# Kernel tuning notes

Measured on AMD Instinct MI355X. Metric: run time of the kernel, lower is better.

## Reference

```python
import jax, jax.numpy as jnp
import numpy as np

D_MODEL = 256
N_HEAD = 8
HEAD_DIM = D_MODEL // N_HEAD
N_TOTAL = 24576
B, T = 64, 512


def setup_inputs() -> dict:
    key = jax.random.key(0)
    ks = jax.random.split(key, 12)
    s = 1.0 / np.sqrt(D_MODEL)
    return {
        "x": jax.random.normal(ks[0], (N_TOTAL, D_MODEL), jnp.float32),
        "Wq": jax.random.uniform(ks[1], (D_MODEL, D_MODEL), jnp.float32, -s, s),
        "bq": jax.random.uniform(ks[2], (D_MODEL,), jnp.float32, -s, s),
        "Wk": jax.random.uniform(ks[3], (D_MODEL, D_MODEL), jnp.float32, -s, s),
        "bk": jax.random.uniform(ks[4], (D_MODEL,), jnp.float32, -s, s),
        "Wv": jax.random.uniform(ks[5], (D_MODEL, D_MODEL), jnp.float32, -s, s),
        "bv": jax.random.uniform(ks[6], (D_MODEL,), jnp.float32, -s, s),
        "Wp": jax.random.uniform(ks[7], (D_MODEL, D_MODEL), jnp.float32, -s, s),
        "bp": jax.random.uniform(ks[8], (D_MODEL,), jnp.float32, -s, s),
        "padpack_index": jax.random.randint(ks[9], (B, T), 0, N_TOTAL, jnp.int64 if jax.config.jax_enable_x64 else jnp.int32),
        "padpack_batch": jax.random.randint(ks[10], (B, T), 0, B, jnp.int32),
        "padpack_inverse_index": jax.random.randint(ks[11], (N_TOTAL,), 0, B * T, jnp.int64 if jax.config.jax_enable_x64 else jnp.int32),
    }


def reference(x, Wq, bq, Wk, bk, Wv, bv, Wp, bp, padpack_index, padpack_batch, padpack_inverse_index):
    # gather ragged tokens into packed [B, T, C]
    xp = x[padpack_index]
    # mask: True where packed slots share the same segment id (matches
    # original masked_fill(batch_i == batch_j, -1e9))
    mask = padpack_batch[:, :, None] == padpack_batch[:, None, :]  # [B,T,T]
    # QKV projections (torch Linear: x @ W.T + b), split heads
    def heads(w, b):
        h = xp @ w.T + b
        return h.reshape(B, T, N_HEAD, HEAD_DIM).transpose(0, 2, 1, 3)  # [B,H,T,D]
    q, k, v = heads(Wq, bq), heads(Wk, bk), heads(Wv, bv)
    att = jnp.einsum("bhtd,bhsd->bhts", q, k) * (1.0 / np.sqrt(HEAD_DIM))
    att = jnp.where(mask[:, None], jnp.float32(-1e9), att)
    att = jax.nn.softmax(att, axis=-1)
    y = jnp.einsum("bhts,bhsd->bhtd", att, v)  # [B,H,T,D]
    y = y.transpose(0, 2, 1, 3).reshape(B, T, D_MODEL)
    y = y @ Wp.T + bp
    # scatter back to ragged layout
    return y.reshape(B * T, D_MODEL)[padpack_inverse_index]
```

## Files before the change

### kernel.cpp

```cpp
#include <hip/hip_runtime.h>


typedef __attribute__((ext_vector_type(8))) short short8;
typedef __attribute__((ext_vector_type(4))) short short4_t;
typedef __attribute__((ext_vector_type(4))) float f32x4;

#define N_TOTAL 24576
#define B_ 64
#define T_ 512
#define DM 256
#define NH 8
#define HD 32
#define F3 768

#define QSCALE 0.25503463f
#define VSP 530

__device__ __forceinline__ unsigned short f2bf(float f) {
  unsigned int u = __float_as_uint(f);
  u += 0x7fffu + ((u >> 16) & 1u);
  return (unsigned short)(u >> 16);
}

__device__ __forceinline__ void gl_lds16(const void* g, void* l) {
  __builtin_amdgcn_global_load_lds(
      (const __attribute__((address_space(1))) unsigned int*)g,
      (__attribute__((address_space(3))) unsigned int*)l, 16, 0, 0);
}

__global__ __launch_bounds__(256) void qkv_gemm(
    const float* __restrict__ x, const int* __restrict__ idx,
    const float* __restrict__ Wq, const float* __restrict__ Wk,
    const float* __restrict__ Wv, const float* __restrict__ bq,
    const float* __restrict__ bk, const float* __restrict__ bv,
    unsigned short* __restrict__ QKVp) {
  __shared__ __align__(16) char Asm[8 * 4096];
  __shared__ __align__(16) char Bsm[3 * 8192];
  int tid = threadIdx.x;
  int lane = tid & 63, w = tid >> 6;
  int i = lane & 15, q = lane >> 4;
  int m0 = blockIdx.x * 64;
  int wn = w * 32;
  int csa = q ^ ((i >> 1) & 3);

  int row = tid >> 2, c = tid & 3;
  int cs0 = c ^ ((row >> 1) & 3);
  int brow1 = 64 + row;
  int cs1 = c ^ ((brow1 >> 1) & 3);
  const float* ax = x + (size_t)idx[m0 + row] * DM;

  auto wrow = [&](int f) -> const float* {
    const float* Wb = (f < 256) ? Wq : ((f < 512) ? Wk : Wv);
    return Wb + (size_t)(f & 255) * DM;
  };

  float4 fb[2][2][2];

  auto issueBloads = [&](int g, int par) {
    int p2 = g >> 3, k2 = g & 7;
    const float* s0 = wrow(p2 * 128 + row) + k2 * 32 + cs0 * 8;
    const float* s1 = wrow(p2 * 128 + brow1) + k2 * 32 + cs1 * 8;
    fb[par][0][0] = *(const float4*)(s0);
    fb[par][0][1] = *(const float4*)(s0 + 4);
    fb[par][1][0] = *(const float4*)(s1);
    fb[par][1][1] = *(const float4*)(s1 + 4);
  };
  auto writeB = [&](int g, int par) {
    char* dst = Bsm + (g % 3) * 8192;
    short8 o0, o1;
    float4 l0 = fb[par][0][0], h0 = fb[par][0][1];
    float4 l1 = fb[par][1][0], h1 = fb[par][1][1];
    o0[0] = (short)f2bf(l0.x); o0[1] = (short)f2bf(l0.y);
    o0[2] = (short)f2bf(l0.z); o0[3] = (short)f2bf(l0.w);
    o0[4] = (short)f2bf(h0.x); o0[5] = (short)f2bf(h0.y);
    o0[6] = (short)f2bf(h0.z); o0[7] = (short)f2bf(h0.w);
    o1[0] = (short)f2bf(l1.x); o1[1] = (short)f2bf(l1.y);
    o1[2] = (short)f2bf(l1.z); o1[3] = (short)f2bf(l1.w);
    o1[4] = (short)f2bf(h1.x); o1[5] = (short)f2bf(h1.y);
    o1[6] = (short)f2bf(h1.z); o1[7] = (short)f2bf(h1.w);
    *(short8*)(dst + tid * 16) = o0;
    *(short8*)(dst + (256 + tid) * 16) = o1;
  };

  issueBloads(0, 0);
  issueBloads(1, 1);
#pragma unroll
  for (int k = 0; k < 8; k++) {
    float4 lo = *(const float4*)(ax + k * 32 + cs0 * 8);
    float4 hi = *(const float4*)(ax + k * 32 + cs0 * 8 + 4);
    short8 o;
    o[0] = (short)f2bf(lo.x); o[1] = (short)f2bf(lo.y);
    o[2] = (short)f2bf(lo.z); o[3] = (short)f2bf(lo.w);
    o[4] = (short)f2bf(hi.x); o[5] = (short)f2bf(hi.y);
    o[6] = (short)f2bf(hi.z); o[7] = (short)f2bf(hi.w);
    *(short8*)(Asm + k * 4096 + tid * 16) = o;
  }
  writeB(0, 0);

  f32x4 zf = {0.f, 0.f, 0.f, 0.f};
  f32x4 acc[4][2];
#pragma unroll
  for (int mt = 0; mt < 4; mt++) {
    acc[mt][0] = zf;
    acc[mt][1] = zf;
  }

#pragma unroll 1
  for (int p = 0; p < 6; p++) {
#pragma unroll
    for (int k = 0; k < 8; k++) {
      int g = p * 8 + k;
      asm volatile("s_waitcnt lgkmcnt(0)\ns_barrier" ::: "memory");
      const short* Asb = (const short*)(Asm + k * 4096);
      const short* Bsb = (const short*)(Bsm + (g % 3) * 8192);
      short8 a[4], bfr[2];
#pragma unroll
      for (int mt = 0; mt < 4; mt++)
        a[mt] = *(const short8*)&Asb[(mt * 16 + i) * 32 + csa * 8];
#pragma unroll
      for (int nt = 0; nt < 2; nt++)
        bfr[nt] = *(const short8*)&Bsb[(wn + nt * 16 + i) * 32 + csa * 8];
      if (g + 2 < 48) issueBloads(g + 2, k & 1);
#pragma unroll
      for (int mt = 0; mt < 4; mt++) {
        acc[mt][0] = __builtin_amdgcn_mfma_f32_16x16x32_bf16(a[mt], bfr[0], acc[mt][0], 0, 0, 0);
        acc[mt][1] = __builtin_amdgcn_mfma_f32_16x16x32_bf16(a[mt], bfr[1], acc[mt][1], 0, 0, 0);
      }
      if (g + 1 < 48) writeB(g + 1, (k + 1) & 1);
    }
    float scale = (p < 2) ? QSCALE : 1.0f;
    const float* bb = (p < 2) ? bq : ((p < 4) ? bk : bv);
    int boff = (p < 2) ? 0 : ((p < 4) ? 256 : 512);
#pragma unroll
    for (int nt = 0; nt < 2; nt++) {
      int f = p * 128 + wn + nt * 16 + i;
      float bias = bb[f - boff];
#pragma unroll
      for (int mt = 0; mt < 4; mt++) {
#pragma unroll
        for (int r = 0; r < 4; r++) {
          int token = m0 + mt * 16 + q * 4 + r;
          QKVp[(size_t)token * F3 + f] = f2bf((acc[mt][nt][r] + bias) * scale);
        }
        acc[mt][nt] = zf;
      }
    }
  }
}

__global__ __launch_bounds__(512, 4) void attn_kernel(
    const unsigned short* __restrict__ QKVp, const int* __restrict__ batch,
    const float* __restrict__ Wp, short* __restrict__ WPb,
    unsigned short* __restrict__ Y) {
  __shared__ __align__(16) short Vl[HD * VSP];
  __shared__ int sbat[T_];
  int tid = threadIdx.x, w = tid >> 6, lane = tid & 63;
  int i = lane & 15, q = lane >> 4;
  int bx = blockIdx.x;
  int h = bx >> 6, b = bx & 63;
  int t0 = w * 64;
  const unsigned short* Tok = QKVp + (size_t)b * T_ * F3;

  sbat[tid] = batch[b * T_ + tid];

  if (bx < 32) {
    int u = bx * 512 + tid;
    float4 v = ((const float4*)Wp)[u];
    short4_t o;
    o[0] = (short)f2bf(v.x); o[1] = (short)f2bf(v.y);
    o[2] = (short)f2bf(v.z); o[3] = (short)f2bf(v.w);
    *(short4_t*)(WPb + (size_t)u * 4) = o;
  }

  {
    int seg = tid & 3, sb = tid >> 2;
#pragma unroll
    for (int l = 0; l < 4; l++) {
      int s = sb + l * 128;
      short8 v = *(const short8*)&Tok[(size_t)s * F3 + 512 + h * HD + seg * 8];
#pragma unroll
      for (int j = 0; j < 8; j++) Vl[(seg * 8 + j) * VSP + s] = v[j];
    }
  }
  __syncthreads();

  short8 qf[4];
  int btm[4];
#pragma unroll
  for (int mt = 0; mt < 4; mt++)
    qf[mt] = *(const short8*)&Tok[(size_t)(t0 + mt * 16 + i) * F3 + h * HD + q * 8];
#pragma unroll
  for (int mt = 0; mt < 4; mt++) btm[mt] = sbat[t0 + mt * 16 + i];

  unsigned short ob = (i == 0) ? (unsigned short)0x3F80 : (unsigned short)0;
  short8 ones = {(short)ob, (short)ob, (short)ob, (short)ob,
                 (short)ob, (short)ob, (short)ob, (short)ob};

  f32x4 zf = {0.f, 0.f, 0.f, 0.f};
  f32x4 o[4][2], lacc[4];
#pragma unroll
  for (int mt = 0; mt < 4; mt++) {
    o[mt][0] = zf; o[mt][1] = zf; lacc[mt] = zf;
  }

  const unsigned short* Kb = Tok + 256 + h * HD + q * 8;
  short8 k0f = *(const short8*)&Kb[(size_t)(i)*F3];
  short8 k1f = *(const short8*)&Kb[(size_t)(16 + i) * F3];

  for (int s0 = 0; s0 < T_; s0 += 32) {
    short8 ck0 = k0f, ck1 = k1f;
    if (s0 + 32 < T_) {
      k0f = *(const short8*)&Kb[(size_t)(s0 + 32 + i) * F3];
      k1f = *(const short8*)&Kb[(size_t)(s0 + 48 + i) * F3];
    }
    int4 bs0 = *(const int4*)&sbat[s0 + q * 4];
    int4 bs1 = *(const int4*)&sbat[s0 + 16 + q * 4];
    short8 v0f = *(const short8*)&Vl[i * VSP + s0 + q * 8];
    short8 v1f = *(const short8*)&Vl[(16 + i) * VSP + s0 + q * 8];
#pragma unroll
    for (int mt = 0; mt < 4; mt++) {
      f32x4 st0 = __builtin_amdgcn_mfma_f32_16x16x32_bf16(ck0, qf[mt], zf, 0, 0, 0);
      f32x4 st1 = __builtin_amdgcn_mfma_f32_16x16x32_bf16(ck1, qf[mt], zf, 0, 0, 0);
      int bm = btm[mt];
      float e00 = __builtin_amdgcn_exp2f((bs0.x == bm) ? -1e9f : st0[0]);
      float e01 = __builtin_amdgcn_exp2f((bs0.y == bm) ? -1e9f : st0[1]);
      float e02 = __builtin_amdgcn_exp2f((bs0.z == bm) ? -1e9f : st0[2]);
      float e03 = __builtin_amdgcn_exp2f((bs0.w == bm) ? -1e9f : st0[3]);
      float e10 = __builtin_amdgcn_exp2f((bs1.x == bm) ? -1e9f : st1[0]);
      float e11 = __builtin_amdgcn_exp2f((bs1.y == bm) ? -1e9f : st1[1]);
      float e12 = __builtin_amdgcn_exp2f((bs1.z == bm) ? -1e9f : st1[2]);
      float e13 = __builtin_amdgcn_exp2f((bs1.w == bm) ? -1e9f : st1[3]);
      unsigned A0 = __builtin_amdgcn_perm(__float_as_uint(e01), __float_as_uint(e00), 0x07060302u);
      unsigned A1 = __builtin_amdgcn_perm(__float_as_uint(e03), __float_as_uint(e02), 0x07060302u);
      unsigned B0 = __builtin_amdgcn_perm(__float_as_uint(e11), __float_as_uint(e10), 0x07060302u);
      unsigned B1 = __builtin_amdgcn_perm(__float_as_uint(e13), __float_as_uint(e12), 0x07060302u);
      asm volatile(
          "s_nop 1\n\t"
          "v_permlane32_swap_b32 %0, %2\n\t"
          "v_permlane32_swap_b32 %1, %3\n\t"
          "s_nop 1\n\t"
          "v_permlane16_swap_b32 %0, %2\n\t"
          "v_permlane16_swap_b32 %1, %3\n\t"
          "s_nop 1"
          : "+v"(A0), "+v"(A1), "+v"(B0), "+v"(B1));
      union {
        unsigned u[4];
        short8 s;
      } cv;
      cv.u[0] = A0;
      cv.u[1] = A1;
      cv.u[2] = B0;
      cv.u[3] = B1;
      short8 pa = cv.s;
      o[mt][0] = __builtin_amdgcn_mfma_f32_16x16x32_bf16(pa, v0f, o[mt][0], 0, 0, 0);
      o[mt][1] = __builtin_amdgcn_mfma_f32_16x16x32_bf16(pa, v1f, o[mt][1], 0, 0, 0);
      lacc[mt] = __builtin_amdgcn_mfma_f32_16x16x32_bf16(pa, ones, lacc[mt], 0, 0, 0);
    }
  }

#pragma unroll
  for (int mt = 0; mt < 4; mt++) {
#pragma unroll
    for (int r = 0; r < 4; r++) {
      float lv = __shfl(lacc[mt][r], lane & 48, 64);
      float inv = __builtin_amdgcn_rcpf(lv);
      size_t yb = ((size_t)b * T_ + t0 + mt * 16 + q * 4 + r) * DM + h * HD;
      Y[yb + i] = f2bf(o[mt][0][r] * inv);
      Y[yb + 16 + i] = f2bf(o[mt][1][r] * inv);
    }
  }
}

__global__ __launch_bounds__(256) void out_gemm(
    const short* __restrict__ Y, const short* __restrict__ WPb,
    const float* __restrict__ bp, const int* __restrict__ inv,
    float* __restrict__ out) {
  __shared__ __align__(16) char smem[3 * 16384];
  int tid = threadIdx.x;
  int lane = tid & 63, w = tid >> 6;
  int i = lane & 15, q = lane >> 4;
  int m0 = blockIdx.x * 128, n0 = blockIdx.y * 128;
  int wm = (w & 1) * 64, wn = (w >> 1) * 64;
  int csa = q ^ ((i >> 1) & 3);

  int iv0 = inv[m0 + (tid >> 2)];
  int iv1 = inv[m0 + 64 + (tid >> 2)];

  f32x4 zf = {0.f, 0.f, 0.f, 0.f};
  f32x4 acc[4][4];
#pragma unroll
  for (int mt = 0; mt < 4; mt++)
#pragma unroll
    for (int nt = 0; nt < 4; nt++) acc[mt][nt] = zf;

  auto stage = [&](int k, int s) {
#pragma unroll
    for (int p = 0; p < 2; p++) {
      int U = p * 256 + tid;
      int row = U >> 2, c = U & 3;
      int cs = c ^ ((row >> 1) & 3);
      int iv = p ? iv1 : iv0;
      gl_lds16(Y + (size_t)iv * DM + k * 32 + cs * 8, smem + s * 16384 + U * 16);
      gl_lds16(WPb + (size_t)(n0 + row) * DM + k * 32 + cs * 8,
               smem + s * 16384 + 8192 + U * 16);
    }
  };

  stage(0, 0);
  stage(1, 1);
#pragma unroll
  for (int k = 0; k < 8; k++) {
    if (k == 7)
      asm volatile("s_waitcnt vmcnt(0) lgkmcnt(0)\ns_barrier" ::: "memory");
    else
      asm volatile("s_waitcnt vmcnt(4) lgkmcnt(0)\ns_barrier" ::: "memory");
    const short* Asb = (const short*)(smem + (k % 3) * 16384);
    const short* Bsb = Asb + 4096;
    short8 a[4], bfr[4];
#pragma unroll
    for (int mt = 0; mt < 4; mt++)
      a[mt] = *(const short8*)&Asb[(wm + mt * 16 + i) * 32 + csa * 8];
#pragma unroll
    for (int nt = 0; nt < 4; nt++)
      bfr[nt] = *(const short8*)&Bsb[(wn + nt * 16 + i) * 32 + csa * 8];
    if (k < 6) stage(k + 2, (k + 2) % 3);
#pragma unroll
    for (int mt = 0; mt < 4; mt++)
#pragma unroll
      for (int nt = 0; nt < 4; nt++)
        acc[mt][nt] = __builtin_amdgcn_mfma_f32_16x16x32_bf16(a[mt], bfr[nt], acc[mt][nt], 0, 0, 0);
  }

#pragma unroll
  for (int nt = 0; nt < 4; nt++) {
    int f = n0 + wn + nt * 16 + i;
    float bias = bp[f];
#pragma unroll
    for (int mt = 0; mt < 4; mt++) {
#pragma unroll
      for (int r = 0; r < 4; r++) {
        int row = m0 + wm + mt * 16 + q * 4 + r;
        out[(size_t)row * DM + f] = acc[mt][nt][r] + bias;
      }
    }
  }
}

extern "C" void kernel_launch(void* const* d_in, const int* in_sizes, int n_in,
                              void* d_out, int out_size, void* d_ws, size_t ws_size,
                              hipStream_t stream) {
  const float* x = (const float*)d_in[0];
  const float* Wq = (const float*)d_in[1];
  const float* bq = (const float*)d_in[2];
  const float* Wk = (const float*)d_in[3];
  const float* bk = (const float*)d_in[4];
  const float* Wv = (const float*)d_in[5];
  const float* bv = (const float*)d_in[6];
  const float* Wp = (const float*)d_in[7];
  const float* bp = (const float*)d_in[8];
  const int* idx = (const int*)d_in[9];
  const int* batch = (const int*)d_in[10];
  const int* inv = (const int*)d_in[11];
  float* out = (float*)d_out;

  char* ws = (char*)d_ws;
  short* WPb = (short*)(ws + 524288);
  unsigned short* QKVp = (unsigned short*)(ws + 2097152);
  unsigned short* Yb = (unsigned short*)(ws + 52428800);

  qkv_gemm<<<512, 256, 0, stream>>>(x, idx, Wq, Wk, Wv, bq, bk, bv, QKVp);
  attn_kernel<<<512, 512, 0, stream>>>(QKVp, batch, Wp, WPb, Yb);
  out_gemm<<<dim3(192, 2), 256, 0, stream>>>((const short*)Yb, WPb, bp, inv, out);
}
```

Baseline: 168.6 us.

## Split QKV GEMM output columns across two wave groups in 512-thread blocks

The QKV projection kernel now launches 512 threads per block, split into two groups of four waves. Each group computes half of the 768 output features (three 128-column panels) against a shared A tile. Each group uses its own double-buffered B staging area, and the gathered A rows are loaded cooperatively by all 512 threads. This halves the serial panel loop per block and raises wave-level parallelism, at the cost of larger blocks with a 4-block occupancy hint and block-wide barriers that now span both groups.

New measurement: 175.6 us. +4.1%, slower.

```diff
diff --git a/kernel.cpp b/kernel.cpp
--- a/kernel.cpp
+++ b/kernel.cpp
@@ -28,26 +28,28 @@
       (__attribute__((address_space(3))) unsigned int*)l, 16, 0, 0);
 }
 
-__global__ __launch_bounds__(256) void qkv_gemm(
+__global__ __launch_bounds__(512, 4) void qkv_gemm(
     const float* __restrict__ x, const int* __restrict__ idx,
     const float* __restrict__ Wq, const float* __restrict__ Wk,
     const float* __restrict__ Wv, const float* __restrict__ bq,
     const float* __restrict__ bk, const float* __restrict__ bv,
     unsigned short* __restrict__ QKVp) {
   __shared__ __align__(16) char Asm[8 * 4096];
-  __shared__ __align__(16) char Bsm[3 * 8192];
+  __shared__ __align__(16) char Bsm[2 * 16384];
   int tid = threadIdx.x;
   int lane = tid & 63, w = tid >> 6;
   int i = lane & 15, q = lane >> 4;
   int m0 = blockIdx.x * 64;
-  int wn = w * 32;
+  int group = w >> 2;
+  int wn = (w & 3) * 32;
   int csa = q ^ ((i >> 1) & 3);
 
-  int row = tid >> 2, c = tid & 3;
-  int cs0 = c ^ ((row >> 1) & 3);
-  int brow1 = 64 + row;
+  int t = tid & 255;
+  int brow0 = t >> 2, c = t & 3;
+  int cs0 = c ^ ((brow0 >> 1) & 3);
+  int brow1 = 64 + brow0;
   int cs1 = c ^ ((brow1 >> 1) & 3);
-  const float* ax = x + (size_t)idx[m0 + row] * DM;
+  char* Bbase = Bsm + group * 16384;
 
   auto wrow = [&](int f) -> const float* {
     const float* Wb = (f < 256) ? Wq : ((f < 512) ? Wk : Wv);
@@ -56,17 +58,17 @@
 
   float4 fb[2][2][2];
 
-  auto issueBloads = [&](int g, int par) {
-    int p2 = g >> 3, k2 = g & 7;
-    const float* s0 = wrow(p2 * 128 + row) + k2 * 32 + cs0 * 8;
+  auto issueBloads = [&](int s, int par) {
+    int p2 = group * 3 + (s >> 3), k2 = s & 7;
+    const float* s0 = wrow(p2 * 128 + brow0) + k2 * 32 + cs0 * 8;
     const float* s1 = wrow(p2 * 128 + brow1) + k2 * 32 + cs1 * 8;
     fb[par][0][0] = *(const float4*)(s0);
     fb[par][0][1] = *(const float4*)(s0 + 4);
     fb[par][1][0] = *(const float4*)(s1);
     fb[par][1][1] = *(const float4*)(s1 + 4);
   };
-  auto writeB = [&](int g, int par) {
-    char* dst = Bsm + (g % 3) * 8192;
+  auto writeB = [&](int s, int par) {
+    char* dst = Bbase + (s & 1) * 8192;
     short8 o0, o1;
     float4 l0 = fb[par][0][0], h0 = fb[par][0][1];
     float4 l1 = fb[par][1][0], h1 = fb[par][1][1];
@@ -78,22 +80,28 @@
     o1[2] = (short)f2bf(l1.z); o1[3] = (short)f2bf(l1.w);
     o1[4] = (short)f2bf(h1.x); o1[5] = (short)f2bf(h1.y);
     o1[6] = (short)f2bf(h1.z); o1[7] = (short)f2bf(h1.w);
-    *(short8*)(dst + tid * 16) = o0;
-    *(short8*)(dst + (256 + tid) * 16) = o1;
+    *(short8*)(dst + t * 16) = o0;
+    *(short8*)(dst + (256 + t) * 16) = o1;
   };
 
   issueBloads(0, 0);
   issueBloads(1, 1);
-#pragma unroll
-  for (int k = 0; k < 8; k++) {
-    float4 lo = *(const float4*)(ax + k * 32 + cs0 * 8);
-    float4 hi = *(const float4*)(ax + k * 32 + cs0 * 8 + 4);
-    short8 o;
-    o[0] = (short)f2bf(lo.x); o[1] = (short)f2bf(lo.y);
-    o[2] = (short)f2bf(lo.z); o[3] = (short)f2bf(lo.w);
-    o[4] = (short)f2bf(hi.x); o[5] = (short)f2bf(hi.y);
-    o[6] = (short)f2bf(hi.z); o[7] = (short)f2bf(hi.w);
-    *(short8*)(Asm + k * 4096 + tid * 16) = o;
+  {
+    int arow = tid >> 3, kk = tid & 7;
+    const float* ax = x + (size_t)idx[m0 + arow] * DM + kk * 32;
+    char* ad = Asm + kk * 4096 + arow * 64;
+#pragma unroll
+    for (int cc = 0; cc < 4; cc++) {
+      int cs = cc ^ ((arow >> 1) & 3);
+      float4 lo = *(const float4*)(ax + cs * 8);
+      float4 hi = *(const float4*)(ax + cs * 8 + 4);
+      short8 o;
+      o[0] = (short)f2bf(lo.x); o[1] = (short)f2bf(lo.y);
+      o[2] = (short)f2bf(lo.z); o[3] = (short)f2bf(lo.w);
+      o[4] = (short)f2bf(hi.x); o[5] = (short)f2bf(hi.y);
+      o[6] = (short)f2bf(hi.z); o[7] = (short)f2bf(hi.w);
+      *(short8*)(ad + cc * 16) = o;
+    }
   }
   writeB(0, 0);
 
@@ -106,13 +114,13 @@
   }
 
 #pragma unroll 1
-  for (int p = 0; p < 6; p++) {
+  for (int pp = 0; pp < 3; pp++) {
 #pragma unroll
     for (int k = 0; k < 8; k++) {
-      int g = p * 8 + k;
+      int s = pp * 8 + k;
       asm volatile("s_waitcnt lgkmcnt(0)\ns_barrier" ::: "memory");
       const short* Asb = (const short*)(Asm + k * 4096);
-      const short* Bsb = (const short*)(Bsm + (g % 3) * 8192);
+      const short* Bsb = (const short*)(Bbase + (s & 1) * 8192);
       short8 a[4], bfr[2];
 #pragma unroll
       for (int mt = 0; mt < 4; mt++)
@@ -120,14 +128,15 @@
 #pragma unroll
       for (int nt = 0; nt < 2; nt++)
         bfr[nt] = *(const short8*)&Bsb[(wn + nt * 16 + i) * 32 + csa * 8];
-      if (g + 2 < 48) issueBloads(g + 2, k & 1);
+      if (s + 2 < 24) issueBloads(s + 2, s & 1);
 #pragma unroll
       for (int mt = 0; mt < 4; mt++) {
         acc[mt][0] = __builtin_amdgcn_mfma_f32_16x16x32_bf16(a[mt], bfr[0], acc[mt][0], 0, 0, 0);
         acc[mt][1] = __builtin_amdgcn_mfma_f32_16x16x32_bf16(a[mt], bfr[1], acc[mt][1], 0, 0, 0);
       }
-      if (g + 1 < 48) writeB(g + 1, (k + 1) & 1);
-    }
+      if (s + 1 < 24) writeB(s + 1, (s + 1) & 1);
+    }
+    int p = group * 3 + pp;
     float scale = (p < 2) ? QSCALE : 1.0f;
     const float* bb = (p < 2) ? bq : ((p < 4) ? bk : bv);
     int boff = (p < 2) ? 0 : ((p < 4) ? 256 : 512);
@@ -368,7 +377,7 @@
   unsigned short* QKVp = (unsigned short*)(ws + 2097152);
   unsigned short* Yb = (unsigned short*)(ws + 52428800);
 
-  qkv_gemm<<<512, 256, 0, stream>>>(x, idx, Wq, Wk, Wv, bq, bk, bv, QKVp);
+  qkv_gemm<<<512, 512, 0, stream>>>(x, idx, Wq, Wk, Wv, bq, bk, bv, QKVp);
   attn_kernel<<<512, 512, 0, stream>>>(QKVp, batch, Wp, WPb, Yb);
   out_gemm<<<dim3(192, 2), 256, 0, stream>>>((const short*)Yb, WPb, bp, inv, out);
 }
```
